# Kernel tuning notes

Hardware: AMD Instinct MI355X
Metric: run time of the kernel (lower is better)

Reference implementation:

```python
import jax, jax.numpy as jnp
import numpy as np

EPS = 1e-5


def setup_inputs() -> dict:
    key = jax.random.key(0)
    k_x, k_y, k_w, k_b = jax.random.split(key, 4)
    B, IN, OUT = 16384, 1024, 1024
    x = jax.random.normal(k_x, (B, IN), dtype=jnp.float32)
    y = jax.random.normal(k_y, (B, OUT), dtype=jnp.float32)
    # nn.Linear default init scale ~ 1/sqrt(in_features); keep activations sane
    weight = jax.random.normal(k_w, (OUT, IN), dtype=jnp.float32) / np.sqrt(IN)
    bias = jax.random.normal(k_b, (OUT,), dtype=jnp.float32) / np.sqrt(IN)
    gamma = jnp.ones((OUT,), dtype=jnp.float32)
    beta = jnp.zeros((OUT,), dtype=jnp.float32)
    return {"x": x, "y": y, "weight": weight, "bias": bias, "gamma": gamma, "beta": beta}


def reference(x, y, weight, bias, gamma, beta):
    # Linear: z[b, o] = sum_i x[b, i] * weight[o, i] + bias[o]
    z = jnp.einsum('bi,oi->bo', x, weight) + bias
    # LayerNorm over the feature (out_features) dim, biased variance
    mean = jnp.mean(z, axis=-1, keepdims=True)
    var = jnp.mean(jnp.square(z), axis=-1, keepdims=True) - jnp.square(mean)
    ln = (z - mean) * jax.lax.rsqrt(var + EPS) * gamma + beta
    # residual add then elementwise multiply
    return (ln + y) * y
```

## Files before the change

### kernel.cpp

```cpp
#include <hip/hip_runtime.h>
#include <stdint.h>

typedef unsigned short u16;
typedef __attribute__((ext_vector_type(8))) short short8;
typedef __attribute__((ext_vector_type(4))) float floatx4;
typedef __attribute__((ext_vector_type(2))) float floatx2;

#define K_DIM 1024
#define N_DIM 1024
#define BK 32
#define NCHUNK 32
#define BM 64
#define HCHUNK 16

__device__ __forceinline__ u16 f2b(float f) {
    union { float f; uint32_t i; } v; v.f = f;
    uint32_t u = v.i;
    return (u16)((u + 0x7FFFu + ((u >> 16) & 1u)) >> 16);
}
__device__ __forceinline__ float b2f(u16 u) {
    union { uint32_t i; float f; } v; v.i = ((uint32_t)u) << 16; return v.f;
}

__global__ __launch_bounds__(256) void pack_w_kernel(const float* __restrict__ w,
                                                     u16* __restrict__ wpk) {
    int gid  = blockIdx.x * 256 + threadIdx.x;
    int lane = gid & 63;
    int kc   = (gid >> 6) & 31;
    int tile = gid >> 11;
    int n = tile * 16 + (lane & 15);
    int k = kc * 32 + (lane >> 4) * 8;
    const float* src = w + (size_t)n * K_DIM + k;
    floatx4 a = *(const floatx4*)(src);
    floatx4 b = *(const floatx4*)(src + 4);
    short8 o;
    o[0] = (short)f2b(a[0]); o[1] = (short)f2b(a[1]);
    o[2] = (short)f2b(a[2]); o[3] = (short)f2b(a[3]);
    o[4] = (short)f2b(b[0]); o[5] = (short)f2b(b[1]);
    o[6] = (short)f2b(b[2]); o[7] = (short)f2b(b[3]);
    *(short8*)(wpk + (size_t)gid * 8) = o;
}

__global__ __launch_bounds__(1024) void gemm256v2_kernel(
    const float* __restrict__ x, const u16* __restrict__ wpk,
    const float* __restrict__ bias, u16* __restrict__ zout,
    float* __restrict__ gsum, float* __restrict__ gsum2)
{
    __shared__ __align__(16) char smem[3 * 32768];
    __shared__ float ls_sum[256];
    __shared__ float ls_sum2[256];

    const int tid  = threadIdx.x;
    const int lane = tid & 63;
    const int wv   = tid >> 6;
    const int wr   = wv >> 2;
    const int wc   = wv & 3;
    const int q    = lane >> 4;
    const int rb   = blockIdx.x & 63;
    const int cb   = blockIdx.x >> 6;
    const int row0 = rb * 256;
    const int col0 = cb * 256;

    if (tid < 256) { ls_sum[tid] = 0.0f; ls_sum2[tid] = 0.0f; }

    const float* xb = x + (size_t)(row0 + (tid >> 2)) * K_DIM + ((tid & 3) << 3);
    const int a_st = wv * 1024 + ((((tid >> 2) & 15) + (tid & 3) * 16) << 4);
    const u16* wb = wpk + ((size_t)(cb * 16 + wv) * 32) * 512 + lane * 8;
    const int b_st = 16384 + wv * 1024 + (lane << 4);

    floatx4 acc[4][4];
#pragma unroll
    for (int mi = 0; mi < 4; ++mi)
#pragma unroll
        for (int ni = 0; ni < 4; ++ni)
            acc[mi][ni] = (floatx4){0.0f, 0.0f, 0.0f, 0.0f};

#pragma unroll
    for (int c = 0; c < 2; ++c) {
        floatx4 a0 = *(const floatx4*)(xb + c * BK);
        floatx4 a1 = *(const floatx4*)(xb + c * BK + 4);
        short8 bv  = *(const short8*)(wb + (size_t)c * 512);
        short8 aw;
        aw[0] = (short)f2b(a0[0]); aw[1] = (short)f2b(a0[1]);
        aw[2] = (short)f2b(a0[2]); aw[3] = (short)f2b(a0[3]);
        aw[4] = (short)f2b(a1[0]); aw[5] = (short)f2b(a1[1]);
        aw[6] = (short)f2b(a1[2]); aw[7] = (short)f2b(a1[3]);
        *(short8*)(smem + c * 32768 + a_st) = aw;
        *(short8*)(smem + c * 32768 + b_st) = bv;
    }
    __syncthreads();

#pragma unroll 1
    for (int kc = 0; kc < NCHUNK; ++kc) {
        const int slot_c = kc % 3;
        const int slot_w = (kc + 2) % 3;
        const bool pf = (kc + 2 < NCHUNK);

        floatx4 a0, a1; short8 bv;
        if (pf) {
            a0 = *(const floatx4*)(xb + (kc + 2) * BK);
            a1 = *(const floatx4*)(xb + (kc + 2) * BK + 4);
            bv = *(const short8*)(wb + (size_t)(kc + 2) * 512);
        }

        const char* As = smem + slot_c * 32768;
        short8 af[4], bf[4];
#pragma unroll
        for (int mi = 0; mi < 4; ++mi)
            af[mi] = *(const short8*)(As + (wr * 4 + mi) * 1024 + (lane << 4));
#pragma unroll
        for (int ni = 0; ni < 4; ++ni)
            bf[ni] = *(const short8*)(As + 16384 + (wc * 4 + ni) * 1024 + (lane << 4));
#pragma unroll
        for (int mi = 0; mi < 4; ++mi)
#pragma unroll
            for (int ni = 0; ni < 4; ++ni)
                acc[mi][ni] = __builtin_amdgcn_mfma_f32_16x16x32_bf16(
                    af[mi], bf[ni], acc[mi][ni], 0, 0, 0);

        if (pf) {
            short8 aw;
            aw[0] = (short)f2b(a0[0]); aw[1] = (short)f2b(a0[1]);
            aw[2] = (short)f2b(a0[2]); aw[3] = (short)f2b(a0[3]);
            aw[4] = (short)f2b(a1[0]); aw[5] = (short)f2b(a1[1]);
            aw[6] = (short)f2b(a1[2]); aw[7] = (short)f2b(a1[3]);
            *(short8*)(smem + slot_w * 32768 + a_st) = aw;
            *(short8*)(smem + slot_w * 32768 + b_st) = bv;
        }

        asm volatile("s_waitcnt lgkmcnt(0)" ::: "memory");
        __builtin_amdgcn_s_barrier();
        asm volatile("" ::: "memory");
    }

    float bias_v[4];
#pragma unroll
    for (int ni = 0; ni < 4; ++ni)
        bias_v[ni] = bias[col0 + wc * 64 + ni * 16 + (lane & 15)];
#pragma unroll
    for (int mi = 0; mi < 4; ++mi)
#pragma unroll
        for (int ni = 0; ni < 4; ++ni)
#pragma unroll
            for (int r = 0; r < 4; ++r)
                acc[mi][ni][r] += bias_v[ni];

#pragma unroll
    for (int mi = 0; mi < 4; ++mi)
#pragma unroll
        for (int r = 0; r < 4; ++r) {
            float s = 0.0f, s2 = 0.0f;
#pragma unroll
            for (int ni = 0; ni < 4; ++ni) {
                float v = acc[mi][ni][r];
                s += v; s2 += v * v;
            }
#pragma unroll
            for (int m = 1; m < 16; m <<= 1) {
                s  += __shfl_xor(s,  m, 64);
                s2 += __shfl_xor(s2, m, 64);
            }
            if ((lane & 15) == 0) {
                int rl = wr * 64 + mi * 16 + (q << 2) + r;
                atomicAdd(&ls_sum[rl], s);
                atomicAdd(&ls_sum2[rl], s2);
            }
        }

    __syncthreads();
    if (tid < 256) {
        atomicAdd(&gsum[row0 + tid],  ls_sum[tid]);
        atomicAdd(&gsum2[row0 + tid], ls_sum2[tid]);
    }

    char* zb = smem;
    for (int s4 = 0; s4 < 4; ++s4) {
        if (wr == s4) {
#pragma unroll
            for (int mi = 0; mi < 4; ++mi)
#pragma unroll
                for (int ni = 0; ni < 4; ++ni)
#pragma unroll
                    for (int r = 0; r < 4; ++r) {
                        int lr  = mi * 16 + (q << 2) + r;
                        int col = wc * 64 + ni * 16 + (lane & 15);
                        int phys = lr * 512 + ((col << 1) ^ (q << 5));
                        *(u16*)(zb + phys) = f2b(acc[mi][ni][r]);
                    }
        }
        __syncthreads();
#pragma unroll
        for (int it = 0; it < 2; ++it) {
            int row = tid >> 4;
            int c8  = (tid & 15) + it * 16;
            int phys = row * 512 + ((c8 << 4) ^ (((row >> 2) & 3) << 5));
            short8 z8 = *(const short8*)(zb + phys);
            *(short8*)(zout + (size_t)(row0 + s4 * 64 + row) * N_DIM + col0 + c8 * 8) = z8;
        }
        __syncthreads();
    }
}

__global__ __launch_bounds__(256) void ln_apply_kernel(
    const u16* __restrict__ z, const float* __restrict__ y,
    const float* __restrict__ stats, const float* __restrict__ gamma,
    const float* __restrict__ beta, float* __restrict__ out)
{
    int g   = blockIdx.x * 256 + threadIdx.x;
    int row = g >> 7;
    int c8  = g & 127;
    float s  = stats[row];
    float s2 = stats[16384 + row];
    float mean = s * (1.0f / 1024.0f);
    float var  = s2 * (1.0f / 1024.0f) - mean * mean;
    float rs   = rsqrtf(var + 1e-5f);
    short8 z8 = *(const short8*)(z + (size_t)row * N_DIM + c8 * 8);
    const float* yp  = y     + (size_t)row * N_DIM + c8 * 8;
    const float* gp  = gamma + c8 * 8;
    const float* bpv = beta  + c8 * 8;
    float*       op  = out   + (size_t)row * N_DIM + c8 * 8;
    floatx4 y0 = *(const floatx4*)(yp);
    floatx4 y1 = *(const floatx4*)(yp + 4);
    floatx4 g0 = *(const floatx4*)(gp);
    floatx4 g1 = *(const floatx4*)(gp + 4);
    floatx4 b0 = *(const floatx4*)(bpv);
    floatx4 b1 = *(const floatx4*)(bpv + 4);
    floatx4 o0, o1;
#pragma unroll
    for (int e = 0; e < 4; ++e) {
        float zv = b2f((u16)z8[e]);
        o0[e] = ((zv - mean) * rs * g0[e] + b0[e] + y0[e]) * y0[e];
    }
#pragma unroll
    for (int e = 0; e < 4; ++e) {
        float zv = b2f((u16)z8[e + 4]);
        o1[e] = ((zv - mean) * rs * g1[e] + b1[e] + y1[e]) * y1[e];
    }
    *(floatx4*)(op)     = o0;
    *(floatx4*)(op + 4) = o1;
}

__global__ __launch_bounds__(1024) void fused_gemm_ln_kernel(
    const float* __restrict__ x, const float* __restrict__ y,
    const u16* __restrict__ wpk, const float* __restrict__ bias,
    const float* __restrict__ gamma, const float* __restrict__ beta,
    float* __restrict__ out)
{
    __shared__ __align__(16) u16 lds16[HCHUNK * BM * BK];
    __shared__ __align__(16) u16 zbuf[16 * 1024];
    __shared__ float ls_sum[64];
    __shared__ float ls_sum2[64];
    __shared__ float ls_mean[64];
    __shared__ float ls_rs[64];

    const int tid  = threadIdx.x;
    const int lane = tid & 63;
    const int wv   = tid >> 6;
    const int q    = lane >> 4;
    const int row0 = blockIdx.x * BM;

    if (tid < 64) { ls_sum[tid] = 0.0f; ls_sum2[tid] = 0.0f; }

    const int sr = tid >> 4;
    const int sk = (tid & 15) << 1;
    const float* s_src = x + (size_t)(row0 + sr) * K_DIM + sk;
    const int s_qs  = (sk >> 3) ^ ((sr >> 1) & 3);
    const int s_off = sr * 64 + s_qs * 16 + (sk & 7) * 2;

    const u16* bp = wpk + (size_t)wv * 65536 + lane * 8;
    const int a_base = (lane & 15) * 64 + (q ^ (((lane & 15) >> 1) & 3)) * 16;

    floatx4 acc[4][4];
#pragma unroll
    for (int mi = 0; mi < 4; ++mi)
#pragma unroll
        for (int ni = 0; ni < 4; ++ni)
            acc[mi][ni] = (floatx4){0.0f, 0.0f, 0.0f, 0.0f};

#pragma unroll 4
    for (int c = 0; c < HCHUNK; ++c) {
        floatx2 v = *(const floatx2*)(s_src + c * BK);
        uint32_t p = (uint32_t)f2b(v[0]) | ((uint32_t)f2b(v[1]) << 16);
        *(uint32_t*)((char*)lds16 + c * 4096 + s_off) = p;
    }
    short8 bfr[2][4];
#pragma unroll
    for (int ni = 0; ni < 4; ++ni)
        bfr[0][ni] = *(const short8*)(bp + ni * 16384);
    __syncthreads();

    for (int half = 0; half < 2; ++half) {
        if (half == 1) {
            __syncthreads();
#pragma unroll 4
            for (int c = 0; c < HCHUNK; ++c) {
                floatx2 v = *(const floatx2*)(s_src + (HCHUNK + c) * BK);
                uint32_t p = (uint32_t)f2b(v[0]) | ((uint32_t)f2b(v[1]) << 16);
                *(uint32_t*)((char*)lds16 + c * 4096 + s_off) = p;
            }
            __syncthreads();
        }
#pragma unroll 2
        for (int c = 0; c < HCHUNK; ++c) {
            const int kc  = half * HCHUNK + c;
            const int cur = kc & 1;
            const int nxt = cur ^ 1;
            const char* ab = (const char*)lds16 + c * 4096;
            short8 af0 = *(const short8*)(ab + a_base);
            short8 af1 = *(const short8*)(ab + a_base + 1024);
            short8 af2 = *(const short8*)(ab + a_base + 2048);
            short8 af3 = *(const short8*)(ab + a_base + 3072);
            const int kn = (kc + 1 < NCHUNK) ? (kc + 1) : kc;
#pragma unroll
            for (int ni = 0; ni < 4; ++ni)
                bfr[nxt][ni] = *(const short8*)(bp + ni * 16384 + kn * 512);
#pragma unroll
            for (int ni = 0; ni < 4; ++ni) {
                acc[0][ni] = __builtin_amdgcn_mfma_f32_16x16x32_bf16(af0, bfr[cur][ni], acc[0][ni], 0, 0, 0);
                acc[1][ni] = __builtin_amdgcn_mfma_f32_16x16x32_bf16(af1, bfr[cur][ni], acc[1][ni], 0, 0, 0);
                acc[2][ni] = __builtin_amdgcn_mfma_f32_16x16x32_bf16(af2, bfr[cur][ni], acc[2][ni], 0, 0, 0);
                acc[3][ni] = __builtin_amdgcn_mfma_f32_16x16x32_bf16(af3, bfr[cur][ni], acc[3][ni], 0, 0, 0);
            }
        }
    }

    float bias_v[4];
#pragma unroll
    for (int ni = 0; ni < 4; ++ni)
        bias_v[ni] = bias[(wv << 6) + (ni << 4) + (lane & 15)];
#pragma unroll
    for (int mi = 0; mi < 4; ++mi)
#pragma unroll
        for (int ni = 0; ni < 4; ++ni)
#pragma unroll
            for (int r = 0; r < 4; ++r)
                acc[mi][ni][r] += bias_v[ni];

    __syncthreads();

#pragma unroll
    for (int mi = 0; mi < 4; ++mi)
#pragma unroll
        for (int r = 0; r < 4; ++r) {
            float s = 0.0f, s2 = 0.0f;
#pragma unroll
            for (int ni = 0; ni < 4; ++ni) {
                float v = acc[mi][ni][r];
                s += v; s2 += v * v;
            }
#pragma unroll
            for (int m = 1; m < 16; m <<= 1) {
                s  += __shfl_xor(s,  m, 64);
                s2 += __shfl_xor(s2, m, 64);
            }
            if ((lane & 15) == 0) {
                int rl = (mi << 4) + (q << 2) + r;
                atomicAdd(&ls_sum[rl], s);
                atomicAdd(&ls_sum2[rl], s2);
            }
        }

    __syncthreads();
    if (tid < 64) {
        float mean = ls_sum[tid] * (1.0f / 1024.0f);
        float var  = ls_sum2[tid] * (1.0f / 1024.0f) - mean * mean;
        ls_mean[tid] = mean;
        ls_rs[tid]   = rsqrtf(var + 1e-5f);
    }

    for (int mi = 0; mi < 4; ++mi) {
#pragma unroll
        for (int ni = 0; ni < 4; ++ni)
#pragma unroll
            for (int r = 0; r < 4; ++r) {
                int lr   = (q << 2) + r;
                int lin  = (((wv << 6) + (ni << 4) + (lane & 15)) << 1);
                int phys = lr * 2048 + (lin ^ (q << 5));
                *(u16*)((char*)zbuf + phys) = f2b(acc[mi][ni][r]);
            }
        __syncthreads();
#pragma unroll
        for (int it = 0; it < 2; ++it) {
            int row  = (tid >> 7) + (it << 3);
            int c8   = tid & 127;
            int phys = row * 2048 + ((c8 << 4) ^ (((row >> 2) & 3) << 5));
            short8 z8 = *(const short8*)((const char*)zbuf + phys);
            int grow  = row0 + (mi << 4) + row;
            float mean = ls_mean[(mi << 4) + row];
            float rs   = ls_rs[(mi << 4) + row];
            const float* yp = y     + (size_t)grow * N_DIM + c8 * 8;
            const float* gp = gamma + c8 * 8;
            const float* bpv = beta + c8 * 8;
            float*       op = out   + (size_t)grow * N_DIM + c8 * 8;
            floatx4 y0 = *(const floatx4*)(yp);
            floatx4 y1 = *(const floatx4*)(yp + 4);
            floatx4 g0 = *(const floatx4*)(gp);
            floatx4 g1 = *(const floatx4*)(gp + 4);
            floatx4 b0 = *(const floatx4*)(bpv);
            floatx4 b1 = *(const floatx4*)(bpv + 4);
            floatx4 o0, o1;
#pragma unroll
            for (int e = 0; e < 4; ++e) {
                float zv = b2f((u16)z8[e]);
                o0[e] = ((zv - mean) * rs * g0[e] + b0[e] + y0[e]) * y0[e];
            }
#pragma unroll
            for (int e = 0; e < 4; ++e) {
                float zv = b2f((u16)z8[e + 4]);
                o1[e] = ((zv - mean) * rs * g1[e] + b1[e] + y1[e]) * y1[e];
            }
            *(floatx4*)(op)     = o0;
            *(floatx4*)(op + 4) = o1;
        }
        __syncthreads();
    }
}

extern "C" void kernel_launch(void* const* d_in, const int* in_sizes, int n_in,
                              void* d_out, int out_size, void* d_ws, size_t ws_size,
                              hipStream_t stream) {
    const float* x     = (const float*)d_in[0];
    const float* y     = (const float*)d_in[1];
    const float* wgt   = (const float*)d_in[2];
    const float* bias  = (const float*)d_in[3];
    const float* gamma = (const float*)d_in[4];
    const float* beta  = (const float*)d_in[5];
    float* out = (float*)d_out;

    u16* wpk = (u16*)d_ws;
    const size_t WPK_BYTES   = 2u * 1024u * 1024u;
    const size_t STATS_BYTES = 128u * 1024u;
    const size_t Z_BYTES     = 32u * 1024u * 1024u;
    const int M = in_sizes[0] / K_DIM;

    pack_w_kernel<<<512, 256, 0, stream>>>(wgt, wpk);

    if (ws_size >= WPK_BYTES + STATS_BYTES + Z_BYTES) {
        float* stats = (float*)((char*)d_ws + WPK_BYTES);
        u16*   zws   = (u16*)((char*)d_ws + WPK_BYTES + STATS_BYTES);
        hipMemsetAsync(stats, 0, STATS_BYTES, stream);
        gemm256v2_kernel<<<(M / 256) * 4, 1024, 0, stream>>>(
            x, wpk, bias, zws, stats, stats + 16384);
        ln_apply_kernel<<<M * (N_DIM / 8) / 256, 256, 0, stream>>>(
            zws, y, stats, gamma, beta, out);
    } else {
        fused_gemm_ln_kernel<<<M / BM, 1024, 0, stream>>>(
            x, y, wpk, bias, gamma, beta, out);
    }
}
```

Baseline: 231.2 us.

## Load weight tiles via direct global-to-LDS DMA and stagger A-tile conversion

The GEMM main loop now moves the packed bf16 weight tiles straight into LDS with global_load_lds instead of going through registers. The fp32 x tile is fetched two chunks ahead and converted and stored one chunk ahead, so the bf16 conversion overlaps with the MFMA block. The MFMA section is wrapped in s_setprio, and vmcnt waits are set to track the outstanding DMA. The aim is to cut VGPR traffic and stall time in the pipeline, at the cost of more delicate wait-count synchronisation.

```diff
diff --git a/kernel.cpp b/kernel.cpp
--- a/kernel.cpp
+++ b/kernel.cpp
@@ -20,6 +20,21 @@
 }
 __device__ __forceinline__ float b2f(u16 u) {
     union { uint32_t i; float f; } v; v.i = ((uint32_t)u) << 16; return v.f;
+}
+
+__device__ __forceinline__ void ldsdma16(const u16* g, char* l) {
+    __builtin_amdgcn_global_load_lds(
+        (const __attribute__((address_space(1))) void*)g,
+        (__attribute__((address_space(3))) void*)l, 16, 0, 0);
+}
+
+__device__ __forceinline__ short8 cvt8(floatx4 a0, floatx4 a1) {
+    short8 aw;
+    aw[0] = (short)f2b(a0[0]); aw[1] = (short)f2b(a0[1]);
+    aw[2] = (short)f2b(a0[2]); aw[3] = (short)f2b(a0[3]);
+    aw[4] = (short)f2b(a1[0]); aw[5] = (short)f2b(a1[1]);
+    aw[6] = (short)f2b(a1[2]); aw[7] = (short)f2b(a1[3]);
+    return aw;
 }
 
 __global__ __launch_bounds__(256) void pack_w_kernel(const float* __restrict__ w,
@@ -33,15 +48,11 @@
     const float* src = w + (size_t)n * K_DIM + k;
     floatx4 a = *(const floatx4*)(src);
     floatx4 b = *(const floatx4*)(src + 4);
-    short8 o;
-    o[0] = (short)f2b(a[0]); o[1] = (short)f2b(a[1]);
-    o[2] = (short)f2b(a[2]); o[3] = (short)f2b(a[3]);
-    o[4] = (short)f2b(b[0]); o[5] = (short)f2b(b[1]);
-    o[6] = (short)f2b(b[2]); o[7] = (short)f2b(b[3]);
+    short8 o = cvt8(a, b);
     *(short8*)(wpk + (size_t)gid * 8) = o;
 }
 
-__global__ __launch_bounds__(1024) void gemm256v2_kernel(
+__global__ __launch_bounds__(1024) void gemm256v3_kernel(
     const float* __restrict__ x, const u16* __restrict__ wpk,
     const float* __restrict__ bias, u16* __restrict__ zout,
     float* __restrict__ gsum, float* __restrict__ gsum2)
@@ -63,10 +74,9 @@
 
     if (tid < 256) { ls_sum[tid] = 0.0f; ls_sum2[tid] = 0.0f; }
 
-    const float* xb = x + (size_t)(row0 + (tid >> 2)) * K_DIM + ((tid & 3) << 3);
-    const int a_st = wv * 1024 + ((((tid >> 2) & 15) + (tid & 3) * 16) << 4);
+    const float* xb = x + (size_t)(row0 + wv * 16 + (lane & 15)) * K_DIM + ((lane >> 4) << 3);
+    const int a_st = wv * 1024 + lane * 16;
     const u16* wb = wpk + ((size_t)(cb * 16 + wv) * 32) * 512 + lane * 8;
-    const int b_st = 16384 + wv * 1024 + (lane << 4);
 
     floatx4 acc[4][4];
 #pragma unroll
@@ -75,60 +85,59 @@
         for (int ni = 0; ni < 4; ++ni)
             acc[mi][ni] = (floatx4){0.0f, 0.0f, 0.0f, 0.0f};
 
-#pragma unroll
-    for (int c = 0; c < 2; ++c) {
-        floatx4 a0 = *(const floatx4*)(xb + c * BK);
-        floatx4 a1 = *(const floatx4*)(xb + c * BK + 4);
-        short8 bv  = *(const short8*)(wb + (size_t)c * 512);
-        short8 aw;
-        aw[0] = (short)f2b(a0[0]); aw[1] = (short)f2b(a0[1]);
-        aw[2] = (short)f2b(a0[2]); aw[3] = (short)f2b(a0[3]);
-        aw[4] = (short)f2b(a1[0]); aw[5] = (short)f2b(a1[1]);
-        aw[6] = (short)f2b(a1[2]); aw[7] = (short)f2b(a1[3]);
-        *(short8*)(smem + c * 32768 + a_st) = aw;
-        *(short8*)(smem + c * 32768 + b_st) = bv;
-    }
+    {
+        floatx4 a0 = *(const floatx4*)(xb);
+        floatx4 a1 = *(const floatx4*)(xb + 4);
+        *(short8*)(smem + a_st) = cvt8(a0, a1);
+    }
+    floatx4 pa0 = *(const floatx4*)(xb + 32);
+    floatx4 pa1 = *(const floatx4*)(xb + 36);
+    ldsdma16(wb,       smem + 0 * 32768 + 16384 + wv * 1024);
+    ldsdma16(wb + 512, smem + 1 * 32768 + 16384 + wv * 1024);
+    asm volatile("s_waitcnt vmcnt(0)" ::: "memory");
     __syncthreads();
 
 #pragma unroll 1
     for (int kc = 0; kc < NCHUNK; ++kc) {
         const int slot_c = kc % 3;
-        const int slot_w = (kc + 2) % 3;
+        const int slot_a = (kc + 1) % 3;
+        const int slot_b = (kc + 2) % 3;
         const bool pf = (kc + 2 < NCHUNK);
-
-        floatx4 a0, a1; short8 bv;
-        if (pf) {
-            a0 = *(const floatx4*)(xb + (kc + 2) * BK);
-            a1 = *(const floatx4*)(xb + (kc + 2) * BK + 4);
-            bv = *(const short8*)(wb + (size_t)(kc + 2) * 512);
-        }
 
         const char* As = smem + slot_c * 32768;
         short8 af[4], bf[4];
 #pragma unroll
         for (int mi = 0; mi < 4; ++mi)
-            af[mi] = *(const short8*)(As + (wr * 4 + mi) * 1024 + (lane << 4));
-#pragma unroll
-        for (int ni = 0; ni < 4; ++ni)
-            bf[ni] = *(const short8*)(As + 16384 + (wc * 4 + ni) * 1024 + (lane << 4));
+            af[mi] = *(const short8*)(As + (wr * 4 + mi) * 1024 + lane * 16);
+#pragma unroll
+        for (int ni = 0; ni < 4; ++ni)
+            bf[ni] = *(const short8*)(As + 16384 + (wc * 4 + ni) * 1024 + lane * 16);
+
+        floatx4 na0, na1;
+        if (pf) {
+            na0 = *(const floatx4*)(xb + (kc + 2) * 32);
+            na1 = *(const floatx4*)(xb + (kc + 2) * 32 + 4);
+            ldsdma16(wb + (size_t)(kc + 2) * 512,
+                     smem + slot_b * 32768 + 16384 + wv * 1024);
+        }
+
+        if (kc + 1 < NCHUNK)
+            *(short8*)(smem + slot_a * 32768 + a_st) = cvt8(pa0, pa1);
+
+        __builtin_amdgcn_s_setprio(1);
 #pragma unroll
         for (int mi = 0; mi < 4; ++mi)
 #pragma unroll
             for (int ni = 0; ni < 4; ++ni)
                 acc[mi][ni] = __builtin_amdgcn_mfma_f32_16x16x32_bf16(
                     af[mi], bf[ni], acc[mi][ni], 0, 0, 0);
-
-        if (pf) {
-            short8 aw;
-            aw[0] = (short)f2b(a0[0]); aw[1] = (short)f2b(a0[1]);
-            aw[2] = (short)f2b(a0[2]); aw[3] = (short)f2b(a0[3]);
-            aw[4] = (short)f2b(a1[0]); aw[5] = (short)f2b(a1[1]);
-            aw[6] = (short)f2b(a1[2]); aw[7] = (short)f2b(a1[3]);
-            *(short8*)(smem + slot_w * 32768 + a_st) = aw;
-            *(short8*)(smem + slot_w * 32768 + b_st) = bv;
-        }
+        __builtin_amdgcn_s_setprio(0);
+
+        if (pf) { pa0 = na0; pa1 = na1; }
 
         asm volatile("s_waitcnt lgkmcnt(0)" ::: "memory");
+        if (pf) asm volatile("s_waitcnt vmcnt(3)" ::: "memory");
+        else    asm volatile("s_waitcnt vmcnt(0)" ::: "memory");
         __builtin_amdgcn_s_barrier();
         asm volatile("" ::: "memory");
     }
@@ -439,7 +448,7 @@
         float* stats = (float*)((char*)d_ws + WPK_BYTES);
         u16*   zws   = (u16*)((char*)d_ws + WPK_BYTES + STATS_BYTES);
         hipMemsetAsync(stats, 0, STATS_BYTES, stream);
-        gemm256v2_kernel<<<(M / 256) * 4, 1024, 0, stream>>>(
+        gemm256v3_kernel<<<(M / 256) * 4, 1024, 0, stream>>>(
             x, wpk, bias, zws, stats, stats + 16384);
         ln_apply_kernel<<<M * (N_DIM / 8) / 256, 256, 0, stream>>>(
             zws, y, stats, gamma, beta, out);
```

Result: faster. 225.1 us (-2.6%).
